# Optimization experiments

Measured on AMD Instinct MI355X. Metric: run time of the kernel, lower is better.

The kernel has to match this reference:

```python
import jax, jax.numpy as jnp
import numpy as np

EMB_DIM = 2048
N_HEADS = 16
HEAD_DIM = EMB_DIM // N_HEADS
B, S = 4, 2048


def setup_inputs() -> dict:
    key = jax.random.key(0)
    kx, kq, kk, kv, ko = jax.random.split(key, 5)
    scale = 0.02
    return {
        "x": jax.random.normal(kx, (B, S, EMB_DIM), dtype=jnp.float32),
        "Wq": jax.random.normal(kq, (EMB_DIM, EMB_DIM), dtype=jnp.float32) * scale,
        "Wk": jax.random.normal(kk, (EMB_DIM, EMB_DIM), dtype=jnp.float32) * scale,
        "Wv": jax.random.normal(kv, (EMB_DIM, EMB_DIM), dtype=jnp.float32) * scale,
        "Wo": jax.random.normal(ko, (EMB_DIM, EMB_DIM), dtype=jnp.float32) * scale,
        "bo": jnp.zeros((EMB_DIM,), dtype=jnp.float32),
    }


def _split_heads(t):
    # [B, S, E] -> [B, H, S, Dh]
    b, s, _ = t.shape
    return t.reshape(b, s, N_HEADS, HEAD_DIM).transpose(0, 2, 1, 3)


def reference(x, Wq, Wk, Wv, Wo, bo):
    # torch nn.Linear: y = x @ W.T (no bias for qkv, bias for out_proj)
    q = _split_heads(x @ Wq.T)  # [B, H, S, Dh]
    k = _split_heads(x @ Wk.T)
    v = _split_heads(x @ Wv.T)

    scores = jnp.einsum("bhqd,bhkd->bhqk", q, k)  # [B, H, S, S]
    q_pos = jnp.arange(S)
    k_pos = jnp.arange(S)
    causal_mask = q_pos[:, None] < k_pos[None, :]  # True => future token, masked
    scores = jnp.where(causal_mask, -jnp.inf, scores)
    attn = jax.nn.softmax(scores / np.sqrt(HEAD_DIM).astype(np.float32), axis=-1)
    # dropout rate 0 (eval) -> identity
    ctx = jnp.einsum("bhqk,bhkd->bhqd", attn, v)  # [B, H, S, Dh]
    ctx = ctx.transpose(0, 2, 1, 3).reshape(B, S, EMB_DIM)
    return ctx @ Wo.T + bo
```

## Files before the change

### kernel.cpp

```cpp
#include <hip/hip_runtime.h>
#include <math.h>

#define EMB 2048
#define HD 128
#define SEQ 2048
#define MTOT 8192

typedef __bf16 bf16x8 __attribute__((ext_vector_type(8)));
typedef float floatx4 __attribute__((ext_vector_type(4)));

__device__ __forceinline__ unsigned short f2bf(float f) {
    unsigned u = __float_as_uint(f);
    return (unsigned short)((u + 0x7FFFu + ((u >> 16) & 1u)) >> 16);
}

__device__ __forceinline__ void gl_lds16(const void* g, void* lds) {
    __builtin_amdgcn_global_load_lds(
        (const __attribute__((address_space(1))) unsigned int*)g,
        (__attribute__((address_space(3))) unsigned int*)lds,
        16, 0, 0);
}

__global__ void cast_kernel(const float* __restrict__ src,
                            unsigned short* __restrict__ dst, int n4) {
    int i = blockIdx.x * blockDim.x + threadIdx.x;
    if (i >= n4) return;
    float4 v = reinterpret_cast<const float4*>(src)[i];
    ushort4 o;
    o.x = f2bf(v.x); o.y = f2bf(v.y); o.z = f2bf(v.z); o.w = f2bf(v.w);
    reinterpret_cast<ushort4*>(dst)[i] = o;
}

template<bool OUT_F32>
__global__ __launch_bounds__(256, 2)
void gemm_bt(const unsigned short* __restrict__ A,
             const unsigned short* __restrict__ Bw,
             void* __restrict__ Cout,
             const float* __restrict__ bias,
             int M, int N, int K)
{
    __shared__ __align__(16) unsigned short sA[128][32];
    __shared__ __align__(16) unsigned short sB[128][32];

    const int tid  = threadIdx.x;
    const int lane = tid & 63;
    const int wave = tid >> 6;
    const int wm = wave >> 1, wn = wave & 1;
    const int col  = lane & 15;
    const int quad = lane >> 4;

    const int m0 = blockIdx.y * 128;
    const int n0 = blockIdx.x * 128;

    floatx4 acc[4][4];
    #pragma unroll
    for (int i = 0; i < 4; i++)
        #pragma unroll
        for (int j = 0; j < 4; j++)
            #pragma unroll
            for (int r = 0; r < 4; r++) acc[i][j][r] = 0.0f;

    for (int k0 = 0; k0 < K; k0 += 32) {
        #pragma unroll
        for (int i = 0; i < 2; i++) {
            int c = tid + i * 256;
            int row = c >> 2, cc = (c & 3) * 8;
            char* ldsA = (char*)sA + (size_t)(i * 256 + wave * 64) * 16;
            char* ldsB = (char*)sB + (size_t)(i * 256 + wave * 64) * 16;
            gl_lds16(A  + (size_t)(m0 + row) * K + k0 + cc, ldsA);
            gl_lds16(Bw + (size_t)(n0 + row) * K + k0 + cc, ldsB);
        }
        __syncthreads();

        bf16x8 af[4], bfr[4];
        #pragma unroll
        for (int mi = 0; mi < 4; mi++)
            af[mi] = *reinterpret_cast<const bf16x8*>(&sA[wm*64 + mi*16 + col][quad*8]);
        #pragma unroll
        for (int ni = 0; ni < 4; ni++)
            bfr[ni] = *reinterpret_cast<const bf16x8*>(&sB[wn*64 + ni*16 + col][quad*8]);

        #pragma unroll
        for (int mi = 0; mi < 4; mi++)
            #pragma unroll
            for (int ni = 0; ni < 4; ni++)
                acc[mi][ni] = __builtin_amdgcn_mfma_f32_16x16x32_bf16(
                                  af[mi], bfr[ni], acc[mi][ni], 0, 0, 0);
        __syncthreads();
    }

    #pragma unroll
    for (int mi = 0; mi < 4; mi++) {
        #pragma unroll
        for (int ni = 0; ni < 4; ni++) {
            #pragma unroll
            for (int r = 0; r < 4; r++) {
                int row = m0 + wm*64 + mi*16 + quad*4 + r;
                int cg  = n0 + wn*64 + ni*16 + col;
                float v = acc[mi][ni][r];
                if (OUT_F32) {
                    float bb = bias ? bias[cg] : 0.0f;
                    reinterpret_cast<float*>(Cout)[(size_t)row * N + cg] = v + bb;
                } else {
                    reinterpret_cast<unsigned short*>(Cout)[(size_t)row * N + cg] = f2bf(v);
                }
            }
        }
    }
}

__global__ __launch_bounds__(256, 2)
void flash_attn(const unsigned short* __restrict__ Q,
                const unsigned short* __restrict__ Kg,
                const unsigned short* __restrict__ Vg,
                unsigned short* __restrict__ O)
{
    __shared__ __align__(16) unsigned short sK[64 * 128];
    __shared__ __align__(16) unsigned short sVt[128][72];
    __shared__ __align__(16) unsigned short sP[4][16 * 72];

    const int tid  = threadIdx.x;
    const int lane = tid & 63;
    const int w    = tid >> 6;
    const int col  = lane & 15;
    const int quad = lane >> 4;

    const int qsb = (SEQ / 128 - 1) - blockIdx.x;
    const int h   = blockIdx.y;
    const int b   = blockIdx.z;

    const int qbase = qsb * 128;
    const size_t rowbase = (size_t)b * SEQ;
    const int hoff = h * HD;

    const int qg0 = qbase + w*32 + col;
    const int qg1 = qg0 + 16;

    bf16x8 qf[2][4];
    {
        const unsigned short* qr0 = Q + (rowbase + qg0) * EMB + hoff;
        const unsigned short* qr1 = Q + (rowbase + qg1) * EMB + hoff;
        #pragma unroll
        for (int ks = 0; ks < 4; ks++) {
            qf[0][ks] = *reinterpret_cast<const bf16x8*>(qr0 + ks*32 + quad*8);
            qf[1][ks] = *reinterpret_cast<const bf16x8*>(qr1 + ks*32 + quad*8);
        }
    }

    floatx4 oacc[2][8];
    #pragma unroll
    for (int g = 0; g < 2; g++)
        #pragma unroll
        for (int ni = 0; ni < 8; ni++)
            #pragma unroll
            for (int r = 0; r < 4; r++) oacc[g][ni][r] = 0.0f;
    float m_i[2] = {-1e30f, -1e30f}, l_i[2] = {0.0f, 0.0f};

    const float scl = 0.08838834764831845f;
    unsigned short* sPw = sP[w];

    const int ktmax = qbase / 64 + 1;
    for (int kt = 0; kt <= ktmax; kt++) {
        const int k0 = kt * 64;
        #pragma unroll
        for (int i = 0; i < 4; i++) {
            int c = tid + i * 256;
            int key = c >> 4;
            int dblk = (c & 15) ^ (key & 7);
            char* ldsK = (char*)sK + (size_t)(i * 256 + w * 64) * 16;
            gl_lds16(Kg + (rowbase + k0 + key) * EMB + hoff + dblk * 8, ldsK);
        }
        {
            int k4 = (tid & 15) * 4;
            int d0 = (tid >> 4) * 8;
            unsigned short va[4][8];
            #pragma unroll
            for (int kk = 0; kk < 4; kk++)
                *reinterpret_cast<int4*>(va[kk]) =
                    *reinterpret_cast<const int4*>(Vg + (rowbase + k0 + k4 + kk) * EMB + hoff + d0);
            #pragma unroll
            for (int j = 0; j < 8; j++) {
                ushort4 o;
                o.x = va[0][j]; o.y = va[1][j]; o.z = va[2][j]; o.w = va[3][j];
                *reinterpret_cast<ushort4*>(&sVt[d0 + j][k4]) = o;
            }
        }
        __syncthreads();

        if (k0 <= qbase + w*32 + 31) {
            floatx4 sc[2][4];
            #pragma unroll
            for (int g = 0; g < 2; g++)
                #pragma unroll
                for (int ni = 0; ni < 4; ni++)
                    #pragma unroll
                    for (int r = 0; r < 4; r++) sc[g][ni][r] = 0.0f;
            #pragma unroll
            for (int ni = 0; ni < 4; ni++) {
                #pragma unroll
                for (int ks = 0; ks < 4; ks++) {
                    int u = (ni*16 + col) * 16 + ((ks*4 + quad) ^ (col & 7));
                    bf16x8 kf = *reinterpret_cast<const bf16x8*>(&sK[u * 8]);
                    sc[0][ni] = __builtin_amdgcn_mfma_f32_16x16x32_bf16(kf, qf[0][ks], sc[0][ni], 0, 0, 0);
                    sc[1][ni] = __builtin_amdgcn_mfma_f32_16x16x32_bf16(kf, qf[1][ks], sc[1][ni], 0, 0, 0);
                }
            }

            const bool need_mask = (k0 + 63 > qbase + w*32);
            bf16x8 pf[2][2];

            #pragma unroll
            for (int g = 0; g < 2; g++) {
                const int qg = (g == 0) ? qg0 : qg1;
                if (need_mask) {
                    #pragma unroll
                    for (int ni = 0; ni < 4; ni++)
                        #pragma unroll
                        for (int r = 0; r < 4; r++) {
                            int key = k0 + ni*16 + quad*4 + r;
                            if (key > qg) sc[g][ni][r] = -1e30f;
                        }
                }
                float mx = -1e30f;
                #pragma unroll
                for (int ni = 0; ni < 4; ni++)
                    #pragma unroll
                    for (int r = 0; r < 4; r++) mx = fmaxf(mx, sc[g][ni][r]);
                mx = fmaxf(mx, __shfl_xor(mx, 16));
                mx = fmaxf(mx, __shfl_xor(mx, 32));
                float mnew  = fmaxf(m_i[g], mx);
                float alpha = __expf((m_i[g] - mnew) * scl);
                float msc   = mnew * scl;
                float rsum  = 0.0f;
                #pragma unroll
                for (int ni = 0; ni < 4; ni++) {
                    float p0 = __expf(sc[g][ni][0] * scl - msc);
                    float p1 = __expf(sc[g][ni][1] * scl - msc);
                    float p2 = __expf(sc[g][ni][2] * scl - msc);
                    float p3 = __expf(sc[g][ni][3] * scl - msc);
                    rsum += (p0 + p1) + (p2 + p3);
                    ushort4 pk;
                    pk.x = f2bf(p0); pk.y = f2bf(p1); pk.z = f2bf(p2); pk.w = f2bf(p3);
                    *reinterpret_cast<ushort4*>(&sPw[col*72 + ni*16 + quad*4]) = pk;
                }
                rsum += __shfl_xor(rsum, 16);
                rsum += __shfl_xor(rsum, 32);
                l_i[g] = l_i[g] * alpha + rsum;
                m_i[g] = mnew;
                #pragma unroll
                for (int ni = 0; ni < 8; ni++)
                    #pragma unroll
                    for (int r = 0; r < 4; r++) oacc[g][ni][r] *= alpha;
                #pragma unroll
                for (int ks = 0; ks < 2; ks++)
                    pf[g][ks] = *reinterpret_cast<const bf16x8*>(&sPw[col*72 + ks*32 + quad*8]);
            }

            #pragma unroll
            for (int ni = 0; ni < 8; ni++) {
                #pragma unroll
                for (int ks = 0; ks < 2; ks++) {
                    bf16x8 vf = *reinterpret_cast<const bf16x8*>(&sVt[ni*16 + col][ks*32 + quad*8]);
                    oacc[0][ni] = __builtin_amdgcn_mfma_f32_16x16x32_bf16(vf, pf[0][ks], oacc[0][ni], 0, 0, 0);
                    oacc[1][ni] = __builtin_amdgcn_mfma_f32_16x16x32_bf16(vf, pf[1][ks], oacc[1][ni], 0, 0, 0);
                }
            }
        }
        __syncthreads();
    }

    #pragma unroll
    for (int g = 0; g < 2; g++) {
        const int qg = (g == 0) ? qg0 : qg1;
        float inv = 1.0f / l_i[g];
        #pragma unroll
        for (int ni = 0; ni < 8; ni++) {
            ushort4 o4;
            o4.x = f2bf(oacc[g][ni][0] * inv);
            o4.y = f2bf(oacc[g][ni][1] * inv);
            o4.z = f2bf(oacc[g][ni][2] * inv);
            o4.w = f2bf(oacc[g][ni][3] * inv);
            *reinterpret_cast<ushort4*>(O + (rowbase + qg) * EMB + hoff + ni*16 + quad*4) = o4;
        }
    }
}

extern "C" void kernel_launch(void* const* d_in, const int* in_sizes, int n_in,
                              void* d_out, int out_size, void* d_ws, size_t ws_size,
                              hipStream_t stream)
{
    const float* x  = (const float*)d_in[0];
    const float* Wq = (const float*)d_in[1];
    const float* Wk = (const float*)d_in[2];
    const float* Wv = (const float*)d_in[3];
    const float* Wo = (const float*)d_in[4];
    const float* bo = (const float*)d_in[5];
    float* out = (float*)d_out;

    unsigned short* ws = (unsigned short*)d_ws;
    const size_t XN = (size_t)MTOT * EMB;
    const size_t WN = (size_t)EMB * EMB;
    unsigned short* xb  = ws;
    unsigned short* wqb = xb  + XN;
    unsigned short* wkb = wqb + WN;
    unsigned short* wvb = wkb + WN;
    unsigned short* wob = wvb + WN;
    unsigned short* qb  = wob + WN;
    unsigned short* kb  = qb  + XN;
    unsigned short* vb  = kb  + XN;
    unsigned short* ctx = xb;

    cast_kernel<<<(int)(XN/4/256), 256, 0, stream>>>(x,  xb,  (int)(XN/4));
    cast_kernel<<<(int)(WN/4/256), 256, 0, stream>>>(Wq, wqb, (int)(WN/4));
    cast_kernel<<<(int)(WN/4/256), 256, 0, stream>>>(Wk, wkb, (int)(WN/4));
    cast_kernel<<<(int)(WN/4/256), 256, 0, stream>>>(Wv, wvb, (int)(WN/4));
    cast_kernel<<<(int)(WN/4/256), 256, 0, stream>>>(Wo, wob, (int)(WN/4));

    dim3 ggrid(EMB / 128, MTOT / 128);
    gemm_bt<false><<<ggrid, 256, 0, stream>>>(xb, wqb, qb, nullptr, MTOT, EMB, EMB);
    gemm_bt<false><<<ggrid, 256, 0, stream>>>(xb, wkb, kb, nullptr, MTOT, EMB, EMB);
    gemm_bt<false><<<ggrid, 256, 0, stream>>>(xb, wvb, vb, nullptr, MTOT, EMB, EMB);

    flash_attn<<<dim3(SEQ / 128, 16, 4), 256, 0, stream>>>(qb, kb, vb, ctx);

    gemm_bt<true><<<ggrid, 256, 0, stream>>>(ctx, wob, out, bo, MTOT, EMB, EMB);
}
```

Baseline: 716.9 us.

## Double-buffer K tiles and prefetch V into registers in flash attention

The K tile is double-buffered in LDS and the next tile is issued via global_load_lds before computing on the current one. The next V tile is loaded into registers during compute and transposed into sVt after a barrier. The aim is to overlap global memory latency with the MFMA work. The cost is extra LDS (a second 16KB K buffer), which may reduce occupancy below 2 blocks per CU, an extra barrier per iteration, and more register pressure from holding the V prefetch.

```diff
diff --git a/kernel.cpp b/kernel.cpp
--- a/kernel.cpp
+++ b/kernel.cpp
@@ -115,7 +115,7 @@
                 const unsigned short* __restrict__ Vg,
                 unsigned short* __restrict__ O)
 {
-    __shared__ __align__(16) unsigned short sK[64 * 128];
+    __shared__ __align__(16) unsigned short sK[2][64 * 128];
     __shared__ __align__(16) unsigned short sVt[128][72];
     __shared__ __align__(16) unsigned short sP[4][16 * 72];
 
@@ -159,35 +159,58 @@
     const float scl = 0.08838834764831845f;
     unsigned short* sPw = sP[w];
 
+    const int vk4 = (tid & 15) * 4;
+    const int vd0 = (tid >> 4) * 8;
+
     const int ktmax = qbase / 64 + 1;
-    for (int kt = 0; kt <= ktmax; kt++) {
-        const int k0 = kt * 64;
+
+    {
         #pragma unroll
         for (int i = 0; i < 4; i++) {
             int c = tid + i * 256;
             int key = c >> 4;
             int dblk = (c & 15) ^ (key & 7);
-            char* ldsK = (char*)sK + (size_t)(i * 256 + w * 64) * 16;
-            gl_lds16(Kg + (rowbase + k0 + key) * EMB + hoff + dblk * 8, ldsK);
-        }
-        {
-            int k4 = (tid & 15) * 4;
-            int d0 = (tid >> 4) * 8;
-            unsigned short va[4][8];
+            char* ldsK = (char*)sK[0] + (size_t)(i * 256 + w * 64) * 16;
+            gl_lds16(Kg + (rowbase + key) * EMB + hoff + dblk * 8, ldsK);
+        }
+        unsigned short va[4][8];
+        #pragma unroll
+        for (int kk = 0; kk < 4; kk++)
+            *reinterpret_cast<int4*>(va[kk]) =
+                *reinterpret_cast<const int4*>(Vg + (rowbase + vk4 + kk) * EMB + hoff + vd0);
+        #pragma unroll
+        for (int j = 0; j < 8; j++) {
+            ushort4 o;
+            o.x = va[0][j]; o.y = va[1][j]; o.z = va[2][j]; o.w = va[3][j];
+            *reinterpret_cast<ushort4*>(&sVt[vd0 + j][vk4]) = o;
+        }
+    }
+    __syncthreads();
+
+    for (int kt = 0; kt <= ktmax; kt++) {
+        const int cur = kt & 1;
+        const bool has_next = (kt < ktmax);
+        unsigned short va[4][8];
+
+        if (has_next) {
+            const int kn = (kt + 1) * 64;
+            #pragma unroll
+            for (int i = 0; i < 4; i++) {
+                int c = tid + i * 256;
+                int key = c >> 4;
+                int dblk = (c & 15) ^ (key & 7);
+                char* ldsK = (char*)sK[1 - cur] + (size_t)(i * 256 + w * 64) * 16;
+                gl_lds16(Kg + (rowbase + kn + key) * EMB + hoff + dblk * 8, ldsK);
+            }
             #pragma unroll
             for (int kk = 0; kk < 4; kk++)
                 *reinterpret_cast<int4*>(va[kk]) =
-                    *reinterpret_cast<const int4*>(Vg + (rowbase + k0 + k4 + kk) * EMB + hoff + d0);
-            #pragma unroll
-            for (int j = 0; j < 8; j++) {
-                ushort4 o;
-                o.x = va[0][j]; o.y = va[1][j]; o.z = va[2][j]; o.w = va[3][j];
-                *reinterpret_cast<ushort4*>(&sVt[d0 + j][k4]) = o;
-            }
-        }
-        __syncthreads();
-
+                    *reinterpret_cast<const int4*>(Vg + (rowbase + kn + vk4 + kk) * EMB + hoff + vd0);
+        }
+
+        const int k0 = kt * 64;
         if (k0 <= qbase + w*32 + 31) {
+            const unsigned short* sKc = sK[cur];
             floatx4 sc[2][4];
             #pragma unroll
             for (int g = 0; g < 2; g++)
@@ -200,7 +223,7 @@
                 #pragma unroll
                 for (int ks = 0; ks < 4; ks++) {
                     int u = (ni*16 + col) * 16 + ((ks*4 + quad) ^ (col & 7));
-                    bf16x8 kf = *reinterpret_cast<const bf16x8*>(&sK[u * 8]);
+                    bf16x8 kf = *reinterpret_cast<const bf16x8*>(&sKc[u * 8]);
                     sc[0][ni] = __builtin_amdgcn_mfma_f32_16x16x32_bf16(kf, qf[0][ks], sc[0][ni], 0, 0, 0);
                     sc[1][ni] = __builtin_amdgcn_mfma_f32_16x16x32_bf16(kf, qf[1][ks], sc[1][ni], 0, 0, 0);
                 }
@@ -266,7 +289,17 @@
                 }
             }
         }
-        __syncthreads();
+
+        if (has_next) {
+            __syncthreads();
+            #pragma unroll
+            for (int j = 0; j < 8; j++) {
+                ushort4 o;
+                o.x = va[0][j]; o.y = va[1][j]; o.z = va[2][j]; o.w = va[3][j];
+                *reinterpret_cast<ushort4*>(&sVt[vd0 + j][vk4]) = o;
+            }
+            __syncthreads();
+        }
     }
 
     #pragma unroll
```

Result: no change. 727.9 us (+1.5%).

## Merge cast and QKV launches, pair causal q-blocks per attention block

Applied to the files above, without the earlier changes.

Five cast launches become one kernel that picks its source by index range. The three QKV projection GEMMs become one launch that selects weights and outputs by blockIdx.z. Flash attention now has each block handle two q-blocks, a long one and its mirror short one, so every block does equal causal work. This halves the attention grid to 512 blocks, which may lower occupancy and latency hiding, in exchange for fewer launches and no tail imbalance.

```diff
diff --git a/kernel.cpp b/kernel.cpp
--- a/kernel.cpp
+++ b/kernel.cpp
@@ -21,26 +21,56 @@
         16, 0, 0);
 }
 
-__global__ void cast_kernel(const float* __restrict__ src,
-                            unsigned short* __restrict__ dst, int n4) {
+__global__ void cast_all_kernel(const float* __restrict__ x,
+                                const float* __restrict__ w0,
+                                const float* __restrict__ w1,
+                                const float* __restrict__ w2,
+                                const float* __restrict__ w3,
+                                unsigned short* __restrict__ xb,
+                                unsigned short* __restrict__ wb0,
+                                unsigned short* __restrict__ wb1,
+                                unsigned short* __restrict__ wb2,
+                                unsigned short* __restrict__ wb3)
+{
+    const int XN4 = MTOT * EMB / 4;
+    const int WN4 = EMB * EMB / 4;
     int i = blockIdx.x * blockDim.x + threadIdx.x;
-    if (i >= n4) return;
-    float4 v = reinterpret_cast<const float4*>(src)[i];
+    const float* src; unsigned short* dst; int off;
+    if (i < XN4) { src = x; dst = xb; off = i; }
+    else {
+        int j = i - XN4;
+        int wsel = j >> 20;
+        off = j & (WN4 - 1);
+        switch (wsel) {
+            case 0: src = w0; dst = wb0; break;
+            case 1: src = w1; dst = wb1; break;
+            case 2: src = w2; dst = wb2; break;
+            default: src = w3; dst = wb3; break;
+        }
+    }
+    float4 v = reinterpret_cast<const float4*>(src)[off];
     ushort4 o;
     o.x = f2bf(v.x); o.y = f2bf(v.y); o.z = f2bf(v.z); o.w = f2bf(v.w);
-    reinterpret_cast<ushort4*>(dst)[i] = o;
+    reinterpret_cast<ushort4*>(dst)[off] = o;
 }
 
 template<bool OUT_F32>
 __global__ __launch_bounds__(256, 2)
 void gemm_bt(const unsigned short* __restrict__ A,
-             const unsigned short* __restrict__ Bw,
-             void* __restrict__ Cout,
+             const unsigned short* __restrict__ Bw0,
+             const unsigned short* __restrict__ Bw1,
+             const unsigned short* __restrict__ Bw2,
+             void* __restrict__ Cout0,
+             void* __restrict__ Cout1,
+             void* __restrict__ Cout2,
              const float* __restrict__ bias,
              int M, int N, int K)
 {
     __shared__ __align__(16) unsigned short sA[128][32];
     __shared__ __align__(16) unsigned short sB[128][32];
+
+    const unsigned short* Bw = (blockIdx.z == 0) ? Bw0 : (blockIdx.z == 1) ? Bw1 : Bw2;
+    void* Cout = (blockIdx.z == 0) ? Cout0 : (blockIdx.z == 1) ? Cout1 : Cout2;
 
     const int tid  = threadIdx.x;
     const int lane = tid & 63;
@@ -125,162 +155,165 @@
     const int col  = lane & 15;
     const int quad = lane >> 4;
 
-    const int qsb = (SEQ / 128 - 1) - blockIdx.x;
-    const int h   = blockIdx.y;
-    const int b   = blockIdx.z;
-
-    const int qbase = qsb * 128;
+    const int h = blockIdx.y;
+    const int b = blockIdx.z;
     const size_t rowbase = (size_t)b * SEQ;
     const int hoff = h * HD;
 
-    const int qg0 = qbase + w*32 + col;
-    const int qg1 = qg0 + 16;
-
-    bf16x8 qf[2][4];
-    {
-        const unsigned short* qr0 = Q + (rowbase + qg0) * EMB + hoff;
-        const unsigned short* qr1 = Q + (rowbase + qg1) * EMB + hoff;
-        #pragma unroll
-        for (int ks = 0; ks < 4; ks++) {
-            qf[0][ks] = *reinterpret_cast<const bf16x8*>(qr0 + ks*32 + quad*8);
-            qf[1][ks] = *reinterpret_cast<const bf16x8*>(qr1 + ks*32 + quad*8);
-        }
-    }
-
-    floatx4 oacc[2][8];
-    #pragma unroll
-    for (int g = 0; g < 2; g++)
-        #pragma unroll
-        for (int ni = 0; ni < 8; ni++)
-            #pragma unroll
-            for (int r = 0; r < 4; r++) oacc[g][ni][r] = 0.0f;
-    float m_i[2] = {-1e30f, -1e30f}, l_i[2] = {0.0f, 0.0f};
-
     const float scl = 0.08838834764831845f;
     unsigned short* sPw = sP[w];
 
-    const int ktmax = qbase / 64 + 1;
-    for (int kt = 0; kt <= ktmax; kt++) {
-        const int k0 = kt * 64;
-        #pragma unroll
-        for (int i = 0; i < 4; i++) {
-            int c = tid + i * 256;
-            int key = c >> 4;
-            int dblk = (c & 15) ^ (key & 7);
-            char* ldsK = (char*)sK + (size_t)(i * 256 + w * 64) * 16;
-            gl_lds16(Kg + (rowbase + k0 + key) * EMB + hoff + dblk * 8, ldsK);
-        }
+    const int vk4 = (tid & 15) * 4;
+    const int vd0 = (tid >> 4) * 8;
+
+    #pragma unroll
+    for (int phase = 0; phase < 2; phase++) {
+        const int qsb = phase ? (int)blockIdx.x : (SEQ/128 - 1) - (int)blockIdx.x;
+        const int qbase = qsb * 128;
+        const int qg0 = qbase + w*32 + col;
+        const int qg1 = qg0 + 16;
+
+        bf16x8 qf[2][4];
         {
-            int k4 = (tid & 15) * 4;
-            int d0 = (tid >> 4) * 8;
-            unsigned short va[4][8];
-            #pragma unroll
-            for (int kk = 0; kk < 4; kk++)
-                *reinterpret_cast<int4*>(va[kk]) =
-                    *reinterpret_cast<const int4*>(Vg + (rowbase + k0 + k4 + kk) * EMB + hoff + d0);
-            #pragma unroll
-            for (int j = 0; j < 8; j++) {
-                ushort4 o;
-                o.x = va[0][j]; o.y = va[1][j]; o.z = va[2][j]; o.w = va[3][j];
-                *reinterpret_cast<ushort4*>(&sVt[d0 + j][k4]) = o;
-            }
-        }
-        __syncthreads();
-
-        if (k0 <= qbase + w*32 + 31) {
-            floatx4 sc[2][4];
-            #pragma unroll
-            for (int g = 0; g < 2; g++)
-                #pragma unroll
-                for (int ni = 0; ni < 4; ni++)
-                    #pragma unroll
-                    for (int r = 0; r < 4; r++) sc[g][ni][r] = 0.0f;
-            #pragma unroll
-            for (int ni = 0; ni < 4; ni++) {
-                #pragma unroll
-                for (int ks = 0; ks < 4; ks++) {
-                    int u = (ni*16 + col) * 16 + ((ks*4 + quad) ^ (col & 7));
-                    bf16x8 kf = *reinterpret_cast<const bf16x8*>(&sK[u * 8]);
-                    sc[0][ni] = __builtin_amdgcn_mfma_f32_16x16x32_bf16(kf, qf[0][ks], sc[0][ni], 0, 0, 0);
-                    sc[1][ni] = __builtin_amdgcn_mfma_f32_16x16x32_bf16(kf, qf[1][ks], sc[1][ni], 0, 0, 0);
-                }
-            }
-
-            const bool need_mask = (k0 + 63 > qbase + w*32);
-            bf16x8 pf[2][2];
-
-            #pragma unroll
-            for (int g = 0; g < 2; g++) {
-                const int qg = (g == 0) ? qg0 : qg1;
-                if (need_mask) {
+            const unsigned short* qr0 = Q + (rowbase + qg0) * EMB + hoff;
+            const unsigned short* qr1 = Q + (rowbase + qg1) * EMB + hoff;
+            #pragma unroll
+            for (int ks = 0; ks < 4; ks++) {
+                qf[0][ks] = *reinterpret_cast<const bf16x8*>(qr0 + ks*32 + quad*8);
+                qf[1][ks] = *reinterpret_cast<const bf16x8*>(qr1 + ks*32 + quad*8);
+            }
+        }
+
+        floatx4 oacc[2][8];
+        #pragma unroll
+        for (int g = 0; g < 2; g++)
+            #pragma unroll
+            for (int ni = 0; ni < 8; ni++)
+                #pragma unroll
+                for (int r = 0; r < 4; r++) oacc[g][ni][r] = 0.0f;
+        float m_i[2] = {-1e30f, -1e30f}, l_i[2] = {0.0f, 0.0f};
+
+        const int ktmax = qbase / 64 + 1;
+        for (int kt = 0; kt <= ktmax; kt++) {
+            const int k0 = kt * 64;
+            #pragma unroll
+            for (int i = 0; i < 4; i++) {
+                int c = tid + i * 256;
+                int key = c >> 4;
+                int dblk = (c & 15) ^ (key & 7);
+                char* ldsK = (char*)sK + (size_t)(i * 256 + w * 64) * 16;
+                gl_lds16(Kg + (rowbase + k0 + key) * EMB + hoff + dblk * 8, ldsK);
+            }
+            {
+                unsigned short va[4][8];
+                #pragma unroll
+                for (int kk = 0; kk < 4; kk++)
+                    *reinterpret_cast<int4*>(va[kk]) =
+                        *reinterpret_cast<const int4*>(Vg + (rowbase + k0 + vk4 + kk) * EMB + hoff + vd0);
+                #pragma unroll
+                for (int j = 0; j < 8; j++) {
+                    ushort4 o;
+                    o.x = va[0][j]; o.y = va[1][j]; o.z = va[2][j]; o.w = va[3][j];
+                    *reinterpret_cast<ushort4*>(&sVt[vd0 + j][vk4]) = o;
+                }
+            }
+            __syncthreads();
+
+            if (k0 <= qbase + w*32 + 31) {
+                floatx4 sc[2][4];
+                #pragma unroll
+                for (int g = 0; g < 2; g++)
                     #pragma unroll
                     for (int ni = 0; ni < 4; ni++)
                         #pragma unroll
-                        for (int r = 0; r < 4; r++) {
-                            int key = k0 + ni*16 + quad*4 + r;
-                            if (key > qg) sc[g][ni][r] = -1e30f;
-                        }
-                }
-                float mx = -1e30f;
-                #pragma unroll
-                for (int ni = 0; ni < 4; ni++)
-                    #pragma unroll
-                    for (int r = 0; r < 4; r++) mx = fmaxf(mx, sc[g][ni][r]);
-                mx = fmaxf(mx, __shfl_xor(mx, 16));
-                mx = fmaxf(mx, __shfl_xor(mx, 32));
-                float mnew  = fmaxf(m_i[g], mx);
-                float alpha = __expf((m_i[g] - mnew) * scl);
-                float msc   = mnew * scl;
-                float rsum  = 0.0f;
+                        for (int r = 0; r < 4; r++) sc[g][ni][r] = 0.0f;
                 #pragma unroll
                 for (int ni = 0; ni < 4; ni++) {
-                    float p0 = __expf(sc[g][ni][0] * scl - msc);
-                    float p1 = __expf(sc[g][ni][1] * scl - msc);
-                    float p2 = __expf(sc[g][ni][2] * scl - msc);
-                    float p3 = __expf(sc[g][ni][3] * scl - msc);
-                    rsum += (p0 + p1) + (p2 + p3);
-                    ushort4 pk;
-                    pk.x = f2bf(p0); pk.y = f2bf(p1); pk.z = f2bf(p2); pk.w = f2bf(p3);
-                    *reinterpret_cast<ushort4*>(&sPw[col*72 + ni*16 + quad*4]) = pk;
-                }
-                rsum += __shfl_xor(rsum, 16);
-                rsum += __shfl_xor(rsum, 32);
-                l_i[g] = l_i[g] * alpha + rsum;
-                m_i[g] = mnew;
-                #pragma unroll
-                for (int ni = 0; ni < 8; ni++)
-                    #pragma unroll
-                    for (int r = 0; r < 4; r++) oacc[g][ni][r] *= alpha;
-                #pragma unroll
-                for (int ks = 0; ks < 2; ks++)
-                    pf[g][ks] = *reinterpret_cast<const bf16x8*>(&sPw[col*72 + ks*32 + quad*8]);
-            }
-
+                    #pragma unroll
+                    for (int ks = 0; ks < 4; ks++) {
+                        int u = (ni*16 + col) * 16 + ((ks*4 + quad) ^ (col & 7));
+                        bf16x8 kf = *reinterpret_cast<const bf16x8*>(&sK[u * 8]);
+                        sc[0][ni] = __builtin_amdgcn_mfma_f32_16x16x32_bf16(kf, qf[0][ks], sc[0][ni], 0, 0, 0);
+                        sc[1][ni] = __builtin_amdgcn_mfma_f32_16x16x32_bf16(kf, qf[1][ks], sc[1][ni], 0, 0, 0);
+                    }
+                }
+
+                const bool need_mask = (k0 + 63 > qbase + w*32);
+                bf16x8 pf[2][2];
+
+                #pragma unroll
+                for (int g = 0; g < 2; g++) {
+                    const int qg = (g == 0) ? qg0 : qg1;
+                    if (need_mask) {
+                        #pragma unroll
+                        for (int ni = 0; ni < 4; ni++)
+                            #pragma unroll
+                            for (int r = 0; r < 4; r++) {
+                                int key = k0 + ni*16 + quad*4 + r;
+                                if (key > qg) sc[g][ni][r] = -1e30f;
+                            }
+                    }
+                    float mx = -1e30f;
+                    #pragma unroll
+                    for (int ni = 0; ni < 4; ni++)
+                        #pragma unroll
+                        for (int r = 0; r < 4; r++) mx = fmaxf(mx, sc[g][ni][r]);
+                    mx = fmaxf(mx, __shfl_xor(mx, 16));
+                    mx = fmaxf(mx, __shfl_xor(mx, 32));
+                    float mnew  = fmaxf(m_i[g], mx);
+                    float alpha = __expf((m_i[g] - mnew) * scl);
+                    float msc   = mnew * scl;
+                    float rsum  = 0.0f;
+                    #pragma unroll
+                    for (int ni = 0; ni < 4; ni++) {
+                        float p0 = __expf(sc[g][ni][0] * scl - msc);
+                        float p1 = __expf(sc[g][ni][1] * scl - msc);
+                        float p2 = __expf(sc[g][ni][2] * scl - msc);
+                        float p3 = __expf(sc[g][ni][3] * scl - msc);
+                        rsum += (p0 + p1) + (p2 + p3);
+                        ushort4 pk;
+                        pk.x = f2bf(p0); pk.y = f2bf(p1); pk.z = f2bf(p2); pk.w = f2bf(p3);
+                        *reinterpret_cast<ushort4*>(&sPw[col*72 + ni*16 + quad*4]) = pk;
+                    }
+                    rsum += __shfl_xor(rsum, 16);
+                    rsum += __shfl_xor(rsum, 32);
+                    l_i[g] = l_i[g] * alpha + rsum;
+                    m_i[g] = mnew;
+                    #pragma unroll
+                    for (int ni = 0; ni < 8; ni++)
+                        #pragma unroll
+                        for (int r = 0; r < 4; r++) oacc[g][ni][r] *= alpha;
+                    #pragma unroll
+                    for (int ks = 0; ks < 2; ks++)
+                        pf[g][ks] = *reinterpret_cast<const bf16x8*>(&sPw[col*72 + ks*32 + quad*8]);
+                }
+
+                #pragma unroll
+                for (int ni = 0; ni < 8; ni++) {
+                    #pragma unroll
+                    for (int ks = 0; ks < 2; ks++) {
+                        bf16x8 vf = *reinterpret_cast<const bf16x8*>(&sVt[ni*16 + col][ks*32 + quad*8]);
+                        oacc[0][ni] = __builtin_amdgcn_mfma_f32_16x16x32_bf16(vf, pf[0][ks], oacc[0][ni], 0, 0, 0);
+                        oacc[1][ni] = __builtin_amdgcn_mfma_f32_16x16x32_bf16(vf, pf[1][ks], oacc[1][ni], 0, 0, 0);
+                    }
+                }
+            }
+            __syncthreads();
+        }
+
+        #pragma unroll
+        for (int g = 0; g < 2; g++) {
+            const int qg = (g == 0) ? qg0 : qg1;
+            float inv = 1.0f / l_i[g];
             #pragma unroll
             for (int ni = 0; ni < 8; ni++) {
-                #pragma unroll
-                for (int ks = 0; ks < 2; ks++) {
-                    bf16x8 vf = *reinterpret_cast<const bf16x8*>(&sVt[ni*16 + col][ks*32 + quad*8]);
-                    oacc[0][ni] = __builtin_amdgcn_mfma_f32_16x16x32_bf16(vf, pf[0][ks], oacc[0][ni], 0, 0, 0);
-                    oacc[1][ni] = __builtin_amdgcn_mfma_f32_16x16x32_bf16(vf, pf[1][ks], oacc[1][ni], 0, 0, 0);
-                }
-            }
-        }
-        __syncthreads();
-    }
-
-    #pragma unroll
-    for (int g = 0; g < 2; g++) {
-        const int qg = (g == 0) ? qg0 : qg1;
-        float inv = 1.0f / l_i[g];
-        #pragma unroll
-        for (int ni = 0; ni < 8; ni++) {
-            ushort4 o4;
-            o4.x = f2bf(oacc[g][ni][0] * inv);
-            o4.y = f2bf(oacc[g][ni][1] * inv);
-            o4.z = f2bf(oacc[g][ni][2] * inv);
-            o4.w = f2bf(oacc[g][ni][3] * inv);
-            *reinterpret_cast<ushort4*>(O + (rowbase + qg) * EMB + hoff + ni*16 + quad*4) = o4;
+                ushort4 o4;
+                o4.x = f2bf(oacc[g][ni][0] * inv);
+                o4.y = f2bf(oacc[g][ni][1] * inv);
+                o4.z = f2bf(oacc[g][ni][2] * inv);
+                o4.w = f2bf(oacc[g][ni][3] * inv);
+                *reinterpret_cast<ushort4*>(O + (rowbase + qg) * EMB + hoff + ni*16 + quad*4) = o4;
+            }
         }
     }
 }
@@ -310,18 +343,17 @@
     unsigned short* vb  = kb  + XN;
     unsigned short* ctx = xb;
 
-    cast_kernel<<<(int)(XN/4/256), 256, 0, stream>>>(x,  xb,  (int)(XN/4));
-    cast_kernel<<<(int)(WN/4/256), 256, 0, stream>>>(Wq, wqb, (int)(WN/4));
-    cast_kernel<<<(int)(WN/4/256), 256, 0, stream>>>(Wk, wkb, (int)(WN/4));
-    cast_kernel<<<(int)(WN/4/256), 256, 0, stream>>>(Wv, wvb, (int)(WN/4));
-    cast_kernel<<<(int)(WN/4/256), 256, 0, stream>>>(Wo, wob, (int)(WN/4));
-
-    dim3 ggrid(EMB / 128, MTOT / 128);
-    gemm_bt<false><<<ggrid, 256, 0, stream>>>(xb, wqb, qb, nullptr, MTOT, EMB, EMB);
-    gemm_bt<false><<<ggrid, 256, 0, stream>>>(xb, wkb, kb, nullptr, MTOT, EMB, EMB);
-    gemm_bt<false><<<ggrid, 256, 0, stream>>>(xb, wvb, vb, nullptr, MTOT, EMB, EMB);
-
-    flash_attn<<<dim3(SEQ / 128, 16, 4), 256, 0, stream>>>(qb, kb, vb, ctx);
-
-    gemm_bt<true><<<ggrid, 256, 0, stream>>>(ctx, wob, out, bo, MTOT, EMB, EMB);
-}
+    {
+        int total4 = (int)(XN/4 + 4*(WN/4));
+        cast_all_kernel<<<total4 / 256, 256, 0, stream>>>(
+            x, Wq, Wk, Wv, Wo, xb, wqb, wkb, wvb, wob);
+    }
+
+    gemm_bt<false><<<dim3(EMB/128, MTOT/128, 3), 256, 0, stream>>>(
+        xb, wqb, wkb, wvb, qb, kb, vb, nullptr, MTOT, EMB, EMB);
+
+    flash_attn<<<dim3(SEQ/128/2, 16, 4), 256, 0, stream>>>(qb, kb, vb, ctx);
+
+    gemm_bt<true><<<dim3(EMB/128, MTOT/128, 1), 256, 0, stream>>>(
+        ctx, wob, nullptr, nullptr, out, nullptr, nullptr, bo, MTOT, EMB, EMB);
+}
```

Result: faster. 621.9 us (-13.2%).
